# Kernel optimization log

Hardware: AMD Instinct MI355X
Metric: run time of the kernel (lower is better)

## Reference

```python
import jax, jax.numpy as jnp
import numpy as np

N = 32       # number of variables (per-var LSTMs)
L = 128      # window length
D = 128      # hidden dim
HEADS = 8
TAU_MAX = 5
ALPHA = 0.7  # attn_decay_alpha
B = 128      # number of time-ordered windows


def setup_inputs() -> dict:
    key = jax.random.key(0)
    ks = jax.random.split(key, 20)
    s = 0.1
    f = lambda k, shape: (jax.random.normal(k, shape, jnp.float32) * s)
    return {
        "X": jax.random.normal(ks[0], (B, L, N), jnp.float32),
        # per-variable encoder LSTM (input size 1): W_ih (N,4D), W_hh (N,4D,D), combined-style biases kept separate
        "enc_Wih": f(ks[1], (N, 4 * D)),
        "enc_Whh": f(ks[2], (N, 4 * D, D)),
        "enc_b": f(ks[3], (N, 4 * D)),            # b_ih + b_hh merged (mathematically identical)
        "pool_w": f(ks[4], (N, D)),
        "pool_b": f(ks[5], (N,)),
        # shared MultiheadAttention params (torch layout: in_proj (3D,D))
        "in_proj_w": f(ks[6], (3 * D, D)),
        "in_proj_b": f(ks[7], (3 * D,)),
        "out_proj_w": f(ks[8], (D, D)),
        "out_proj_b": f(ks[9], (D,)),
        # per-variable decoder: init_h/init_c Linear(d,d), LSTM(1,d) (input is all-zeros so W_ih drops out), out Linear(d,1)
        "dec_initH_w": f(ks[10], (N, D, D)),
        "dec_initH_b": f(ks[11], (N, D)),
        "dec_initC_w": f(ks[12], (N, D, D)),
        "dec_initC_b": f(ks[13], (N, D)),
        "dec_Whh": f(ks[14], (N, 4 * D, D)),
        "dec_bih": f(ks[15], (N, 4 * D)),
        "dec_bhh": f(ks[16], (N, 4 * D)),
        "dec_out_w": f(ks[17], (N, D)),
        "dec_out_b": f(ks[18], (N,)),
    }


def _lstm_cell(gates, c):
    # torch gate order: i, f, g, o
    i, fg, g, o = jnp.split(gates, 4, axis=-1)
    i = jax.nn.sigmoid(i); fg = jax.nn.sigmoid(fg)
    g = jnp.tanh(g); o = jax.nn.sigmoid(o)
    c = fg * c + i * g
    h = o * jnp.tanh(c)
    return h, c


def _encode(X, Wih, Whh, b, pool_w, pool_b):
    # X: (B,L,N); encoder consumes first L-1 steps of each variable, batched over all N vars
    x = jnp.transpose(X[:, :-1, :], (1, 2, 0))  # (T, N, B)
    Bn = X.shape[0]
    h0 = jnp.zeros((N, Bn, D), X.dtype)

    def step(carry, x_t):  # x_t: (N,B)
        h, c = carry
        gates = (x_t[..., None] * Wih[:, None, :]
                 + jnp.einsum('nbd,ngd->nbg', h, Whh)
                 + b[:, None, :])
        h, c = _lstm_cell(gates, c)
        return (h, c), h

    _, H = jax.lax.scan(step, (h0, h0), x)  # H: (T,N,B,D)
    # TemporalAttnPool: softmax over time of a linear score, weighted sum
    scores = jnp.einsum('tnbd,nd->tnb', H, pool_w) + pool_b[None, :, None]
    a = jax.nn.softmax(scores, axis=0)
    C = jnp.einsum('tnb,tnbd->bnd', a, H)  # (B,N,D)
    return C


def _mha(Q, KV, in_w, in_b, out_w, out_b):
    dh = D // HEADS
    q = Q @ in_w[:D].T + in_b[:D]
    k = KV @ in_w[D:2 * D].T + in_b[D:2 * D]
    v = KV @ in_w[2 * D:].T + in_b[2 * D:]
    sp = lambda x: x.reshape(x.shape[0], x.shape[1], HEADS, dh)
    q, k, v = sp(q), sp(k), sp(v)
    scores = jnp.einsum('bqhd,bkhd->bhqk', q, k) / float(np.sqrt(dh))
    attn = jax.nn.softmax(scores, axis=-1)
    o = jnp.einsum('bhqk,bkhd->bqhd', attn, v).reshape(Q.shape)
    return o @ out_w.T + out_b


def _cross_attend(C, in_w, in_b, out_w, out_b):
    Bn = C.shape[0]
    tmax = min(TAU_MAX, Bn - 1)
    if tmax <= 0:
        return C
    out_sum = jnp.zeros_like(C)
    w_sum = jnp.zeros((Bn, 1, 1), C.dtype)
    for tau in range(1, tmax + 1):  # small fixed loop over lags
        o = _mha(C[tau:], C[:-tau], in_w, in_b, out_w, out_b)
        w = float(np.exp(-ALPHA * (tau - 1)))  # attn_agg == 'decay'
        out_sum = out_sum.at[tau:].add(o * w)
        w_sum = w_sum.at[tau:].add(w)
    out = out_sum / jnp.clip(w_sum, 1e-8)
    return C + out  # residual=True


def _decode(C_star, iHw, iHb, iCw, iCb, Whh, bih, bhh, ow, ob):
    # h0/c0 from tanh(Linear(c_star)); LSTM input is all-zeros so input term reduces to b_ih
    h0 = jnp.tanh(jnp.einsum('bnd,ned->nbe', C_star, iHw) + iHb[:, None, :])
    c0 = jnp.tanh(jnp.einsum('bnd,ned->nbe', C_star, iCw) + iCb[:, None, :])
    b = (bih + bhh)[:, None, :]  # (N,1,4D)

    def step(carry, _):
        h, c = carry
        gates = jnp.einsum('nbd,ngd->nbg', h, Whh) + b
        h, c = _lstm_cell(gates, c)
        o = jnp.einsum('nbd,nd->nb', h, ow) + ob[:, None]
        return (h, c), o

    _, O = jax.lax.scan(step, (h0, c0), None, length=L)  # (L,N,B)
    recon = jnp.transpose(O[:L - 1], (2, 0, 1))  # (B,L-1,N)
    pred = O[L - 1].T                            # (B,N)
    return recon, pred


def reference(X, enc_Wih, enc_Whh, enc_b, pool_w, pool_b,
              in_proj_w, in_proj_b, out_proj_w, out_proj_b,
              dec_initH_w, dec_initH_b, dec_initC_w, dec_initC_b,
              dec_Whh, dec_bih, dec_bhh, dec_out_w, dec_out_b):
    C = _encode(X, enc_Wih, enc_Whh, enc_b, pool_w, pool_b)
    C_star = _cross_attend(C, in_proj_w, in_proj_b, out_proj_w, out_proj_b)
    recon, pred = _decode(C_star, dec_initH_w, dec_initH_b, dec_initC_w, dec_initC_b,
                          dec_Whh, dec_bih, dec_bhh, dec_out_w, dec_out_b)
    return recon, pred, C_star
```

## Files before the change

### kernel.cpp

```cpp
#include <hip/hip_runtime.h>
#include <hip/hip_bf16.h>

typedef unsigned short ushort_t;
typedef unsigned int uint_t;

#define DD   128
#define G4   512
#define BT   16
#define NB   128
#define NV   32

#define OFF_WIH   0
#define OFF_EB    16384
#define OFF_PW    32768
#define OFF_PB    36864
#define OFF_INW   36896
#define OFF_INB   86048
#define OFF_OUTW  86432
#define OFF_OUTB  102816
#define OFF_IHB   102944
#define OFF_ICB   107040
#define OFF_DBIH  111136
#define OFF_DBHH  127520
#define OFF_DOW   143904
#define OFF_DOB   148000
#define P_TOTAL   148032

typedef __attribute__((ext_vector_type(8))) short bf16x8;
typedef __attribute__((ext_vector_type(4))) float f32x4;

__device__ __forceinline__ float bf2f(ushort_t u) {
    union { uint_t i; float f; } x; x.i = ((uint_t)u) << 16; return x.f;
}
__device__ __forceinline__ ushort_t f2bf(float f) {
    __hip_bfloat16 h = __float2bfloat16(f);
    return *(ushort_t*)&h;
}
__device__ __forceinline__ uint_t f2u(float f) {
    union { float f; uint_t i; } x; x.f = f; return x.i;
}
__device__ __forceinline__ float u2f(uint_t u) {
    union { uint_t i; float f; } x; x.i = u; return x.f;
}
__device__ __forceinline__ float sigmoid_f(float x) {
    return __builtin_amdgcn_rcpf(1.f + __expf(-x));
}
__device__ __forceinline__ float tanh_f(float x) {
    float e = __expf(2.f * x);
    return 1.f - 2.f * __builtin_amdgcn_rcpf(e + 1.f);
}
__device__ __forceinline__ float swz_bcast_l15(float v) {
    return u2f((uint_t)__builtin_amdgcn_ds_swizzle((int)f2u(v), 0x000F));
}
__device__ __forceinline__ void store_out(void* out, long idx, float v, int bf) {
    if (bf) ((ushort_t*)out)[idx] = f2bf(v);
    else    ((float*)out)[idx]    = v;
}

struct Ptr19 { const void* p[19]; int e[19]; };

__global__ __launch_bounds__(64) void probe_kernel(Ptr19 a, int* __restrict__ flags) {
    int i = blockIdx.x;
    int t = threadIdx.x;
    int cap = a.e[i] < 2048 ? a.e[i] : 2048;
    int cnt = 0, tot = 0;
    const ushort_t* p = (const ushort_t*)a.p[i];
    for (int j = t; j < cap; j += 64) {
        ushort_t u = p[j];
        float af = fabsf(bf2f(u));
        tot++;
        if (u == 0 || (af > 1e-7f && af < 100.f)) cnt++;
    }
    #pragma unroll
    for (int off = 32; off >= 1; off >>= 1) {
        cnt += __shfl_xor(cnt, off);
        tot += __shfl_xor(tot, off);
    }
    if (t == 0) flags[i] = (cnt * 10 >= tot * 9) ? 1 : 0;
}

__global__ __launch_bounds__(256) void conv_all(Ptr19 a, const int* __restrict__ flags,
                                                float* __restrict__ P) {
    int i = blockIdx.x * 256 + threadIdx.x;
    if (i >= P_TOTAL) return;
    int src, off;
    if      (i < OFF_EB)   { src = 1;  off = i - OFF_WIH; }
    else if (i < OFF_PW)   { src = 3;  off = i - OFF_EB; }
    else if (i < OFF_PB)   { src = 4;  off = i - OFF_PW; }
    else if (i < OFF_INW)  { src = 5;  off = i - OFF_PB; }
    else if (i < OFF_INB)  { src = 6;  off = i - OFF_INW; }
    else if (i < OFF_OUTW) { src = 7;  off = i - OFF_INB; }
    else if (i < OFF_OUTB) { src = 8;  off = i - OFF_OUTW; }
    else if (i < OFF_IHB)  { src = 9;  off = i - OFF_OUTB; }
    else if (i < OFF_ICB)  { src = 11; off = i - OFF_IHB; }
    else if (i < OFF_DBIH) { src = 13; off = i - OFF_ICB; }
    else if (i < OFF_DBHH) { src = 15; off = i - OFF_DBIH; }
    else if (i < OFF_DOW)  { src = 16; off = i - OFF_DBHH; }
    else if (i < OFF_DOB)  { src = 17; off = i - OFF_DOW; }
    else                   { src = 18; off = i - OFF_DOB; }
    int bf = flags[src];
    P[i] = bf ? bf2f(((const ushort_t*)a.p[src])[off]) : ((const float*)a.p[src])[off];
}

__global__ __launch_bounds__(256) void transpose_X(const void* __restrict__ src,
                                                   const int* __restrict__ flags,
                                                   float* __restrict__ Xc) {
    __shared__ float tile[32][65];
    int bt  = blockIdx.x * 32;
    int tn0 = blockIdx.y * 64;
    int bf = flags[0];
    int tx = threadIdx.x & 63, ty = threadIdx.x >> 6;
    #pragma unroll
    for (int k = 0; k < 8; k++) {
        int row = ty * 8 + k;
        int idx = (bt + row) * 4096 + tn0 + tx;
        tile[row][tx] = bf ? bf2f(((const ushort_t*)src)[idx]) : ((const float*)src)[idx];
    }
    __syncthreads();
    int bx = threadIdx.x & 31, tyy = threadIdx.x >> 5;
    #pragma unroll
    for (int k = 0; k < 8; k++) {
        int tn = tn0 + tyy * 8 + k;
        int t = tn >> 5, nn = tn & 31;
        Xc[t * 4096 + nn * 128 + bt + bx] = tile[bx][tyy * 8 + k];
    }
}

__global__ __launch_bounds__(512, 2) void enc_kernel(
    const float* __restrict__ Xc, const void* __restrict__ Wraw,
    const int* __restrict__ flags, const float* __restrict__ P,
    float* __restrict__ Cout)
{
    const int n = blockIdx.y, b0 = blockIdx.x * BT;
    const int tid = threadIdx.x;
    const int w = tid >> 6, lane = tid & 63;
    const int l15 = lane & 15, quad = lane >> 4;
    const int wbf = flags[2];
    const int bown = b0 + l15;

    __shared__ alignas(16) ushort_t hS[2][16 * 136];
    for (int i = tid; i < 16 * 136; i += 512) hS[0][i] = 0;

    bf16x8 afrag[4][4];
    #pragma unroll
    for (int typ = 0; typ < 4; typ++) {
        const int g = typ * 128 + 16 * w + l15;
        #pragma unroll
        for (int kc = 0; kc < 4; kc++) {
            const int base = (n * G4 + g) * DD + 32 * kc + 8 * quad;
            if (wbf) {
                afrag[typ][kc] = *(const bf16x8*)((const ushort_t*)Wraw + base);
            } else {
                const float* fp = (const float*)Wraw + base;
                bf16x8 tmp;
                #pragma unroll
                for (int j = 0; j < 8; j++) tmp[j] = (short)f2bf(fp[j]);
                afrag[typ][kc] = tmp;
            }
        }
    }

    bf16x8 pfrag[4];
    #pragma unroll
    for (int kc = 0; kc < 4; kc++) {
        bf16x8 tmp;
        #pragma unroll
        for (int j = 0; j < 8; j++)
            tmp[j] = (l15 == 0 || l15 == 8)
                   ? (short)f2bf(P[OFF_PW + n * DD + 32 * kc + 8 * quad + j]) : (short)0;
        pfrag[kc] = tmp;
    }

    f32x4 bias4[4], wih4[4];
    #pragma unroll
    for (int typ = 0; typ < 4; typ++) {
        int base = n * G4 + typ * 128 + 16 * w + 4 * quad;
        bias4[typ] = *(const f32x4*)&P[OFF_EB + base];
        wih4[typ]  = *(const f32x4*)&P[OFF_WIH + base];
    }
    const float pb_r = P[OFF_PB + n];

    float cst[4], hprev[4], Cacc[4], lR = 0.f;
    #pragma unroll
    for (int r = 0; r < 4; r++) { cst[r] = 0.f; hprev[r] = 0.f; Cacc[r] = 0.f; }

    float xq = Xc[n * 128 + bown];

#define ENC_STEP(T, RB)                                                              \
    do {                                                                             \
        __syncthreads();                                                             \
        bf16x8 bh[4];                                                                \
        _Pragma("unroll")                                                            \
        for (int kc = 0; kc < 4; kc++)                                               \
            bh[kc] = *(const bf16x8*)&hS[RB][l15 * 136 + 32 * kc + 8 * quad];        \
        f32x4 acc[4], accP;                                                          \
        _Pragma("unroll")                                                            \
        for (int typ = 0; typ < 4; typ++) {                                          \
            f32x4 a;                                                                 \
            a.x = bias4[typ].x + xq * wih4[typ].x;                                   \
            a.y = bias4[typ].y + xq * wih4[typ].y;                                   \
            a.z = bias4[typ].z + xq * wih4[typ].z;                                   \
            a.w = bias4[typ].w + xq * wih4[typ].w;                                   \
            acc[typ] = a;                                                            \
        }                                                                            \
        accP.x = pb_r; accP.y = pb_r; accP.z = pb_r; accP.w = pb_r;                  \
        if ((T) < 126) xq = Xc[((T) + 1) * 4096 + n * 128 + bown];                   \
        _Pragma("unroll")                                                            \
        for (int kc = 0; kc < 4; kc++) {                                             \
            accP = __builtin_amdgcn_mfma_f32_16x16x32_bf16(pfrag[kc], bh[kc], accP, 0, 0, 0); \
            _Pragma("unroll")                                                        \
            for (int typ = 0; typ < 4; typ++)                                        \
                acc[typ] = __builtin_amdgcn_mfma_f32_16x16x32_bf16(afrag[typ][kc], bh[kc], acc[typ], 0, 0, 0); \
        }                                                                            \
        if ((T) > 0) {                                                               \
            float e = __expf(swz_bcast_l15(accP[0]));                                \
            lR += e;                                                                 \
            _Pragma("unroll")                                                        \
            for (int r = 0; r < 4; r++) Cacc[r] = fmaf(e, hprev[r], Cacc[r]);        \
        }                                                                            \
        ushort4 hw;                                                                  \
        _Pragma("unroll")                                                            \
        for (int r = 0; r < 4; r++) {                                                \
            float ii = sigmoid_f(acc[0][r]);                                         \
            float ff = sigmoid_f(acc[1][r]);                                         \
            float g2 = tanh_f(acc[2][r]);                                            \
            float oo = sigmoid_f(acc[3][r]);                                         \
            float cc = ff * cst[r] + ii * g2;                                        \
            cst[r] = cc;                                                             \
            float hh = oo * tanh_f(cc);                                              \
            hprev[r] = hh;                                                           \
            ((ushort_t*)&hw)[r] = f2bf(hh);                                          \
        }                                                                            \
        *(ushort4*)&hS[(RB) ^ 1][l15 * 136 + 16 * w + 4 * quad] = hw;                \
    } while (0)

    for (int tp = 0; tp < 63; tp++) {
        ENC_STEP(2 * tp, 0);
        ENC_STEP(2 * tp + 1, 1);
    }
    ENC_STEP(126, 0);
#undef ENC_STEP

    __syncthreads();
    {
        f32x4 accP;
        accP.x = pb_r; accP.y = pb_r; accP.z = pb_r; accP.w = pb_r;
        #pragma unroll
        for (int kc = 0; kc < 4; kc++) {
            bf16x8 bh = *(const bf16x8*)&hS[1][l15 * 136 + 32 * kc + 8 * quad];
            accP = __builtin_amdgcn_mfma_f32_16x16x32_bf16(pfrag[kc], bh, accP, 0, 0, 0);
        }
        float e = __expf(swz_bcast_l15(accP[0]));
        lR += e;
        #pragma unroll
        for (int r = 0; r < 4; r++) Cacc[r] = fmaf(e, hprev[r], Cacc[r]);
    }
    float inv = 1.f / lR;
    f32x4 cv;
    cv.x = Cacc[0] * inv; cv.y = Cacc[1] * inv; cv.z = Cacc[2] * inv; cv.w = Cacc[3] * inv;
    *(f32x4*)&Cout[bown * (NV * DD) + n * DD + 16 * w + 4 * quad] = cv;
}

__global__ __launch_bounds__(256) void qkv_kernel(
    const float* __restrict__ C, const float* __restrict__ P,
    float* __restrict__ q, float* __restrict__ k, float* __restrict__ v)
{
    int b = blockIdx.x, p = blockIdx.y, tid = threadIdx.x;
    int j = tid & 127, half = tid >> 7;
    __shared__ float Cb[NV * DD];
    for (int i = tid; i < NV * DD; i += 256) Cb[i] = C[b * (NV * DD) + i];
    __syncthreads();

    const float* wrow = P + OFF_INW + (p * DD + j) * DD;
    float bias = P[OFF_INB + p * DD + j];
    float acc[16];
    #pragma unroll
    for (int nn = 0; nn < 16; nn++) acc[nn] = bias;

    for (int dc = 0; dc < DD; dc += 8) {
        float4 w0 = *(const float4*)&wrow[dc];
        float4 w1 = *(const float4*)&wrow[dc + 4];
        #pragma unroll
        for (int nn = 0; nn < 16; nn++) {
            const float* cb = &Cb[(half * 16 + nn) * DD + dc];
            float4 c0 = *(float4*)&cb[0];
            float4 c1 = *(float4*)&cb[4];
            acc[nn] += c0.x * w0.x + c0.y * w0.y + c0.z * w0.z + c0.w * w0.w
                     + c1.x * w1.x + c1.y * w1.y + c1.z * w1.z + c1.w * w1.w;
        }
    }
    float* dst = (p == 0) ? q : (p == 1) ? k : v;
    for (int nn = 0; nn < 16; nn++)
        dst[b * (NV * DD) + (half * 16 + nn) * DD + j] = acc[nn];
}

__global__ __launch_bounds__(256) void attn_kernel(
    const float* __restrict__ q, const float* __restrict__ k, const float* __restrict__ v,
    const float* __restrict__ C, const float* __restrict__ P,
    const int* __restrict__ flags, float* __restrict__ Cstar, void* __restrict__ dout)
{
    int b = blockIdx.x, tid = threadIdx.x;
    int obf = flags[0];
    __shared__ float Qs[NV * DD], Ks[NV * DD], Vs[NV * DD];
    float* Os = Ks;
    for (int i = tid; i < NV * DD; i += 256) Qs[i] = q[b * (NV * DD) + i];
    __syncthreads();

    int hh = tid >> 5, qi = tid & 31;
    float qreg[16];
    #pragma unroll
    for (int u = 0; u < 4; u++) {
        float4 t4 = *(float4*)&Qs[qi * DD + hh * 16 + 4 * u];
        qreg[4*u] = t4.x; qreg[4*u+1] = t4.y; qreg[4*u+2] = t4.z; qreg[4*u+3] = t4.w;
    }

    float Oacc[16];
    #pragma unroll
    for (int u = 0; u < 16; u++) Oacc[u] = 0.f;
    float wsum = 0.f;
    int tmax = (b < 5) ? b : 5;

    for (int tau = 1; tau <= tmax; tau++) {
        __syncthreads();
        for (int i = tid; i < NV * DD; i += 256) {
            Ks[i] = k[(b - tau) * (NV * DD) + i];
            Vs[i] = v[(b - tau) * (NV * DD) + i];
        }
        __syncthreads();

        float s[NV];
        #pragma unroll
        for (int kk = 0; kk < NV; kk++) {
            float a = 0.f;
            #pragma unroll
            for (int u = 0; u < 4; u++) {
                float4 kv = *(float4*)&Ks[kk * DD + hh * 16 + 4 * u];
                a += qreg[4*u] * kv.x + qreg[4*u+1] * kv.y
                   + qreg[4*u+2] * kv.z + qreg[4*u+3] * kv.w;
            }
            s[kk] = a * 0.25f;
        }
        float mm = s[0];
        #pragma unroll
        for (int kk = 1; kk < NV; kk++) mm = fmaxf(mm, s[kk]);
        float ssum = 0.f;
        #pragma unroll
        for (int kk = 0; kk < NV; kk++) { s[kk] = __expf(s[kk] - mm); ssum += s[kk]; }
        float wdk = __expf(-0.7f * (float)(tau - 1));
        wsum += wdk;
        float wr = wdk / ssum;
        #pragma unroll
        for (int u = 0; u < 4; u++) {
            float ax = 0.f, ay = 0.f, az = 0.f, aw = 0.f;
            #pragma unroll
            for (int kk = 0; kk < NV; kk++) {
                float4 vv = *(float4*)&Vs[kk * DD + hh * 16 + 4 * u];
                ax += s[kk] * vv.x; ay += s[kk] * vv.y;
                az += s[kk] * vv.z; aw += s[kk] * vv.w;
            }
            Oacc[4*u] += wr * ax; Oacc[4*u+1] += wr * ay;
            Oacc[4*u+2] += wr * az; Oacc[4*u+3] += wr * aw;
        }
    }

    __syncthreads();
    float winv = (b > 0) ? 1.f / wsum : 0.f;
    #pragma unroll
    for (int u = 0; u < 16; u++)
        Os[qi * DD + hh * 16 + u] = Oacc[u] * winv;
    __syncthreads();

    int j = tid & 127, ng = tid >> 7;
    const float* wrow = P + OFF_OUTW + j * DD;
    float obias = P[OFF_OUTB + j];
    for (int nn = ng * 16; nn < ng * 16 + 16; nn++) {
        float a = (b > 0) ? obias : 0.f;
        for (int dc = 0; dc < DD; dc += 8) {
            float4 w0 = *(const float4*)&wrow[dc];
            float4 w1 = *(const float4*)&wrow[dc + 4];
            float4 o0 = *(float4*)&Os[nn * DD + dc];
            float4 o1 = *(float4*)&Os[nn * DD + dc + 4];
            a += o0.x*w0.x + o0.y*w0.y + o0.z*w0.z + o0.w*w0.w
               + o1.x*w1.x + o1.y*w1.y + o1.z*w1.z + o1.w*w1.w;
        }
        float cs = C[b * (NV * DD) + nn * DD + j] + a;
        Cstar[b * (NV * DD) + nn * DD + j] = cs;
        store_out(dout, 524288 + b * (NV * DD) + nn * DD + j, cs, obf);
    }
}

__global__ __launch_bounds__(512, 2) void dec_kernel(
    const float* __restrict__ Cstar,
    const void* __restrict__ iHw, const void* __restrict__ iCw,
    const void* __restrict__ Wraw, const int* __restrict__ flags,
    const float* __restrict__ P, void* __restrict__ out)
{
    const int n = blockIdx.y, b0 = blockIdx.x * BT;
    const int tid = threadIdx.x;
    const int w = tid >> 6, lane = tid & 63;
    const int l15 = lane & 15, quad = lane >> 4;
    const int wbf = flags[14], obf = flags[0];
    const int bown = b0 + l15;

    __shared__ alignas(16) ushort_t hS[2][16 * 136];

    bf16x8 cstB[4];
    #pragma unroll
    for (int kc = 0; kc < 4; kc++) {
        const float* cp = &Cstar[bown * (NV * DD) + n * DD + 32 * kc + 8 * quad];
        f32x4 c0v = *(const f32x4*)&cp[0];
        f32x4 c1v = *(const f32x4*)&cp[4];
        bf16x8 tmp;
        tmp[0] = (short)f2bf(c0v.x); tmp[1] = (short)f2bf(c0v.y);
        tmp[2] = (short)f2bf(c0v.z); tmp[3] = (short)f2bf(c0v.w);
        tmp[4] = (short)f2bf(c1v.x); tmp[5] = (short)f2bf(c1v.y);
        tmp[6] = (short)f2bf(c1v.z); tmp[7] = (short)f2bf(c1v.w);
        cstB[kc] = tmp;
    }
    float cst[4];
    {
        const int hbf = flags[10], cbf = flags[12];
        f32x4 hAcc = *(const f32x4*)&P[OFF_IHB + n * DD + 16 * w + 4 * quad];
        f32x4 cAcc = *(const f32x4*)&P[OFF_ICB + n * DD + 16 * w + 4 * quad];
        #pragma unroll
        for (int kc = 0; kc < 4; kc++) {
            const int base = (n * DD + 16 * w + l15) * DD + 32 * kc + 8 * quad;
            bf16x8 wA;
            if (hbf) wA = *(const bf16x8*)((const ushort_t*)iHw + base);
            else {
                const float* fp = (const float*)iHw + base;
                #pragma unroll
                for (int j = 0; j < 8; j++) wA[j] = (short)f2bf(fp[j]);
            }
            hAcc = __builtin_amdgcn_mfma_f32_16x16x32_bf16(wA, cstB[kc], hAcc, 0, 0, 0);
            if (cbf) wA = *(const bf16x8*)((const ushort_t*)iCw + base);
            else {
                const float* fp = (const float*)iCw + base;
                #pragma unroll
                for (int j = 0; j < 8; j++) wA[j] = (short)f2bf(fp[j]);
            }
            cAcc = __builtin_amdgcn_mfma_f32_16x16x32_bf16(wA, cstB[kc], cAcc, 0, 0, 0);
        }
        ushort4 hw;
        #pragma unroll
        for (int r = 0; r < 4; r++) {
            ((ushort_t*)&hw)[r] = f2bf(tanh_f(hAcc[r]));
            cst[r] = tanh_f(cAcc[r]);
        }
        *(ushort4*)&hS[0][l15 * 136 + 16 * w + 4 * quad] = hw;
    }

    bf16x8 afrag[4][4];
    #pragma unroll
    for (int typ = 0; typ < 4; typ++) {
        const int g = typ * 128 + 16 * w + l15;
        #pragma unroll
        for (int kc = 0; kc < 4; kc++) {
            const int base = (n * G4 + g) * DD + 32 * kc + 8 * quad;
            if (wbf) {
                afrag[typ][kc] = *(const bf16x8*)((const ushort_t*)Wraw + base);
            } else {
                const float* fp = (const float*)Wraw + base;
                bf16x8 tmp;
                #pragma unroll
                for (int j = 0; j < 8; j++) tmp[j] = (short)f2bf(fp[j]);
                afrag[typ][kc] = tmp;
            }
        }
    }

    bf16x8 pfrag[4];
    #pragma unroll
    for (int kc = 0; kc < 4; kc++) {
        bf16x8 tmp;
        #pragma unroll
        for (int j = 0; j < 8; j++)
            tmp[j] = (l15 == 0) ? (short)f2bf(P[OFF_DOW + n * DD + 32 * kc + 8 * quad + j]) : (short)0;
        pfrag[kc] = tmp;
    }

    f32x4 bias4[4];
    #pragma unroll
    for (int typ = 0; typ < 4; typ++) {
        int base = n * G4 + typ * 128 + 16 * w + 4 * quad;
        f32x4 b1 = *(const f32x4*)&P[OFF_DBIH + base];
        f32x4 b2 = *(const f32x4*)&P[OFF_DBHH + base];
        bias4[typ].x = b1.x + b2.x; bias4[typ].y = b1.y + b2.y;
        bias4[typ].z = b1.z + b2.z; bias4[typ].w = b1.w + b2.w;
    }
    const float ob_r = P[OFF_DOB + n];

#define DEC_STEP(T, RB)                                                              \
    do {                                                                             \
        __syncthreads();                                                             \
        bf16x8 bh[4];                                                                \
        _Pragma("unroll")                                                            \
        for (int kc = 0; kc < 4; kc++)                                               \
            bh[kc] = *(const bf16x8*)&hS[RB][l15 * 136 + 32 * kc + 8 * quad];        \
        f32x4 acc[4];                                                                \
        _Pragma("unroll")                                                            \
        for (int typ = 0; typ < 4; typ++) acc[typ] = bias4[typ];                     \
        _Pragma("unroll")                                                            \
        for (int kc = 0; kc < 4; kc++)                                               \
            _Pragma("unroll")                                                        \
            for (int typ = 0; typ < 4; typ++)                                        \
                acc[typ] = __builtin_amdgcn_mfma_f32_16x16x32_bf16(afrag[typ][kc], bh[kc], acc[typ], 0, 0, 0); \
        if (w == 0) {                                                                \
            f32x4 accP;                                                              \
            accP.x = ob_r; accP.y = ob_r; accP.z = ob_r; accP.w = ob_r;              \
            _Pragma("unroll")                                                        \
            for (int kc = 0; kc < 4; kc++)                                           \
                accP = __builtin_amdgcn_mfma_f32_16x16x32_bf16(pfrag[kc], bh[kc], accP, 0, 0, 0); \
            if ((T) > 0 && quad == 0)                                                \
                store_out(out, (long)bown * 4064 + (long)((T) - 1) * NV + n, accP[0], obf); \
        }                                                                            \
        ushort4 hw;                                                                  \
        _Pragma("unroll")                                                            \
        for (int r = 0; r < 4; r++) {                                                \
            float ii = sigmoid_f(acc[0][r]);                                         \
            float ff = sigmoid_f(acc[1][r]);                                         \
            float g2 = tanh_f(acc[2][r]);                                            \
            float oo = sigmoid_f(acc[3][r]);                                         \
            float cc = ff * cst[r] + ii * g2;                                        \
            cst[r] = cc;                                                             \
            ((ushort_t*)&hw)[r] = f2bf(oo * tanh_f(cc));                             \
        }                                                                            \
        *(ushort4*)&hS[(RB) ^ 1][l15 * 136 + 16 * w + 4 * quad] = hw;                \
    } while (0)

    for (int tp = 0; tp < 64; tp++) {
        DEC_STEP(2 * tp, 0);
        DEC_STEP(2 * tp + 1, 1);
    }
#undef DEC_STEP

    __syncthreads();
    if (w == 0) {
        f32x4 accP;
        accP.x = ob_r; accP.y = ob_r; accP.z = ob_r; accP.w = ob_r;
        #pragma unroll
        for (int kc = 0; kc < 4; kc++) {
            bf16x8 bh = *(const bf16x8*)&hS[0][l15 * 136 + 32 * kc + 8 * quad];
            accP = __builtin_amdgcn_mfma_f32_16x16x32_bf16(pfrag[kc], bh, accP, 0, 0, 0);
        }
        if (quad == 0)
            store_out(out, 520192 + (long)bown * NV + n, accP[0], obf);
    }
}

extern "C" void kernel_launch(void* const* d_in, const int* in_sizes, int n_in,
                              void* d_out, int out_size, void* d_ws, size_t ws_size,
                              hipStream_t stream) {
    char* ws = (char*)d_ws;
    float*    P    = (float*)(ws + 0);
    float*    Xc   = (float*)(ws + (1u << 20));
    float*    C    = (float*)(ws + (3u << 20));
    float*    qb   = (float*)(ws + (5u << 20));
    float*    kb   = (float*)(ws + (7u << 20));
    float*    vb   = (float*)(ws + (9u << 20));
    float*    Cst  = (float*)(ws + (11u << 20));
    int*      flags = (int*)(ws + (13u << 20));

    Ptr19 a;
    for (int i = 0; i < 19; i++) { a.p[i] = d_in[i]; a.e[i] = in_sizes[i]; }
    probe_kernel<<<19, 64, 0, stream>>>(a, flags);
    conv_all<<<(P_TOTAL + 255) / 256, 256, 0, stream>>>(a, flags, P);
    transpose_X<<<dim3(4, 64), 256, 0, stream>>>(d_in[0], flags, Xc);

    enc_kernel<<<dim3(8, 32), 512, 0, stream>>>(Xc, d_in[2], flags, P, C);
    qkv_kernel<<<dim3(128, 3), 256, 0, stream>>>(C, P, qb, kb, vb);
    attn_kernel<<<dim3(128), 256, 0, stream>>>(qb, kb, vb, C, P, flags, Cst, d_out);
    dec_kernel<<<dim3(8, 32), 512, 0, stream>>>(Cst, d_in[10], d_in[12], d_in[14], flags, P, d_out);
}
```

Before: 435.3 us.

## Fuse prep kernels, move QKV projection into encoder, and merge LSTM cell reciprocals

Merges the probe, parameter-conversion and X-transpose kernels into one prep kernel. Each kernel now detects the input dtype itself with a per-wave probe instead of reading a flags buffer. The QKV projection is folded into the encoder epilogue, working from a shared-memory copy of C, so the separate qkv kernel launch is removed. The LSTM cell shares reciprocals across gate pairs to cut rcp instructions on the recurrent critical path. The cost is redundant probing reads in every block and a scalar-FMA QKV stage inside the encoder.

```diff
diff --git a/kernel.cpp b/kernel.cpp
--- a/kernel.cpp
+++ b/kernel.cpp
@@ -14,17 +14,17 @@
 #define OFF_EB    16384
 #define OFF_PW    32768
 #define OFF_PB    36864
-#define OFF_INW   36896
-#define OFF_INB   86048
-#define OFF_OUTW  86432
-#define OFF_OUTB  102816
-#define OFF_IHB   102944
-#define OFF_ICB   107040
-#define OFF_DBIH  111136
-#define OFF_DBHH  127520
-#define OFF_DOW   143904
-#define OFF_DOB   148000
-#define P_TOTAL   148032
+#define OFF_INW   37120
+#define OFF_INB   86272
+#define OFF_OUTW  86784
+#define OFF_OUTB  103168
+#define OFF_IHB   103424
+#define OFF_ICB   107520
+#define OFF_DBIH  111616
+#define OFF_DBHH  128000
+#define OFF_DOW   144384
+#define OFF_DOB   148480
+#define P_TOTAL   148736
 
 typedef __attribute__((ext_vector_type(8))) short bf16x8;
 typedef __attribute__((ext_vector_type(4))) float f32x4;
@@ -42,13 +42,26 @@
 __device__ __forceinline__ float u2f(uint_t u) {
     union { uint_t i; float f; } x; x.i = u; return x.f;
 }
-__device__ __forceinline__ float sigmoid_f(float x) {
-    return __builtin_amdgcn_rcpf(1.f + __expf(-x));
-}
 __device__ __forceinline__ float tanh_f(float x) {
     float e = __expf(2.f * x);
     return 1.f - 2.f * __builtin_amdgcn_rcpf(e + 1.f);
 }
+__device__ __forceinline__ float lstm_cell(float gi, float gf, float gg, float go, float& c) {
+    float ei = __expf(-gi), ef = __expf(-gf);
+    float di = 1.f + ei, df = 1.f + ef;
+    float r1 = __builtin_amdgcn_rcpf(di * df);
+    float ii = df * r1;
+    float ff = di * r1;
+    float eg = __expf(-2.f * gg), eo = __expf(-go);
+    float dg = 1.f + eg, dz = 1.f + eo;
+    float r2 = __builtin_amdgcn_rcpf(dg * dz);
+    float oo = dg * r2;
+    float tg = (1.f - eg) * (dz * r2);
+    c = ff * c + ii * tg;
+    float ec = __expf(-2.f * c);
+    float tc = (1.f - ec) * __builtin_amdgcn_rcpf(1.f + ec);
+    return oo * tc;
+}
 __device__ __forceinline__ float swz_bcast_l15(float v) {
     return u2f((uint_t)__builtin_amdgcn_ds_swizzle((int)f2u(v), 0x000F));
 }
@@ -56,89 +69,89 @@
     if (bf) ((ushort_t*)out)[idx] = f2bf(v);
     else    ((float*)out)[idx]    = v;
 }
-
-struct Ptr19 { const void* p[19]; int e[19]; };
-
-__global__ __launch_bounds__(64) void probe_kernel(Ptr19 a, int* __restrict__ flags) {
-    int i = blockIdx.x;
-    int t = threadIdx.x;
-    int cap = a.e[i] < 2048 ? a.e[i] : 2048;
+__device__ __forceinline__ int wave_probe(const void* p, int elems) {
+    int cap = elems < 2048 ? elems : 2048;
+    int lane = threadIdx.x & 63;
+    const ushort_t* u = (const ushort_t*)p;
     int cnt = 0, tot = 0;
-    const ushort_t* p = (const ushort_t*)a.p[i];
-    for (int j = t; j < cap; j += 64) {
-        ushort_t u = p[j];
-        float af = fabsf(bf2f(u));
+    for (int j = lane; j < cap; j += 64) {
+        ushort_t x = u[j];
+        float af = fabsf(bf2f(x));
         tot++;
-        if (u == 0 || (af > 1e-7f && af < 100.f)) cnt++;
+        if (x == 0 || (af > 1e-7f && af < 100.f)) cnt++;
     }
     #pragma unroll
     for (int off = 32; off >= 1; off >>= 1) {
         cnt += __shfl_xor(cnt, off);
         tot += __shfl_xor(tot, off);
     }
-    if (t == 0) flags[i] = (cnt * 10 >= tot * 9) ? 1 : 0;
-}
-
-__global__ __launch_bounds__(256) void conv_all(Ptr19 a, const int* __restrict__ flags,
-                                                float* __restrict__ P) {
-    int i = blockIdx.x * 256 + threadIdx.x;
-    if (i >= P_TOTAL) return;
-    int src, off;
-    if      (i < OFF_EB)   { src = 1;  off = i - OFF_WIH; }
-    else if (i < OFF_PW)   { src = 3;  off = i - OFF_EB; }
-    else if (i < OFF_PB)   { src = 4;  off = i - OFF_PW; }
-    else if (i < OFF_INW)  { src = 5;  off = i - OFF_PB; }
-    else if (i < OFF_INB)  { src = 6;  off = i - OFF_INW; }
-    else if (i < OFF_OUTW) { src = 7;  off = i - OFF_INB; }
-    else if (i < OFF_OUTB) { src = 8;  off = i - OFF_OUTW; }
-    else if (i < OFF_IHB)  { src = 9;  off = i - OFF_OUTB; }
-    else if (i < OFF_ICB)  { src = 11; off = i - OFF_IHB; }
-    else if (i < OFF_DBIH) { src = 13; off = i - OFF_ICB; }
-    else if (i < OFF_DBHH) { src = 15; off = i - OFF_DBIH; }
-    else if (i < OFF_DOW)  { src = 16; off = i - OFF_DBHH; }
-    else if (i < OFF_DOB)  { src = 17; off = i - OFF_DOW; }
-    else                   { src = 18; off = i - OFF_DOB; }
-    int bf = flags[src];
-    P[i] = bf ? bf2f(((const ushort_t*)a.p[src])[off]) : ((const float*)a.p[src])[off];
-}
-
-__global__ __launch_bounds__(256) void transpose_X(const void* __restrict__ src,
-                                                   const int* __restrict__ flags,
+    return (cnt * 10 >= tot * 9) ? 1 : 0;
+}
+
+struct Ptr19 { const void* p[19]; };
+
+__global__ __launch_bounds__(256) void prep_kernel(Ptr19 a, float* __restrict__ P,
                                                    float* __restrict__ Xc) {
     __shared__ float tile[32][65];
-    int bt  = blockIdx.x * 32;
-    int tn0 = blockIdx.y * 64;
-    int bf = flags[0];
-    int tx = threadIdx.x & 63, ty = threadIdx.x >> 6;
-    #pragma unroll
-    for (int k = 0; k < 8; k++) {
-        int row = ty * 8 + k;
-        int idx = (bt + row) * 4096 + tn0 + tx;
-        tile[row][tx] = bf ? bf2f(((const ushort_t*)src)[idx]) : ((const float*)src)[idx];
-    }
-    __syncthreads();
-    int bx = threadIdx.x & 31, tyy = threadIdx.x >> 5;
-    #pragma unroll
-    for (int k = 0; k < 8; k++) {
-        int tn = tn0 + tyy * 8 + k;
-        int t = tn >> 5, nn = tn & 31;
-        Xc[t * 4096 + nn * 128 + bt + bx] = tile[bx][tyy * 8 + k];
+    if (blockIdx.x < 581) {
+        int base = blockIdx.x * 256;
+        int src, o0, size;
+        if      (base < OFF_EB)   { src = 1;  o0 = base - OFF_WIH;  size = 16384; }
+        else if (base < OFF_PW)   { src = 3;  o0 = base - OFF_EB;   size = 16384; }
+        else if (base < OFF_PB)   { src = 4;  o0 = base - OFF_PW;   size = 4096;  }
+        else if (base < OFF_INW)  { src = 5;  o0 = base - OFF_PB;   size = 32;    }
+        else if (base < OFF_INB)  { src = 6;  o0 = base - OFF_INW;  size = 49152; }
+        else if (base < OFF_OUTW) { src = 7;  o0 = base - OFF_INB;  size = 384;   }
+        else if (base < OFF_OUTB) { src = 8;  o0 = base - OFF_OUTW; size = 16384; }
+        else if (base < OFF_IHB)  { src = 9;  o0 = base - OFF_OUTB; size = 128;   }
+        else if (base < OFF_ICB)  { src = 11; o0 = base - OFF_IHB;  size = 4096;  }
+        else if (base < OFF_DBIH) { src = 13; o0 = base - OFF_ICB;  size = 4096;  }
+        else if (base < OFF_DBHH) { src = 15; o0 = base - OFF_DBIH; size = 16384; }
+        else if (base < OFF_DOW)  { src = 16; o0 = base - OFF_DBHH; size = 16384; }
+        else if (base < OFF_DOB)  { src = 17; o0 = base - OFF_DOW;  size = 4096;  }
+        else                      { src = 18; o0 = base - OFF_DOB;  size = 32;    }
+        int bf = wave_probe(a.p[src], size);
+        int off = o0 + (int)threadIdx.x;
+        if (off < size)
+            P[base + threadIdx.x] = bf ? bf2f(((const ushort_t*)a.p[src])[off])
+                                       : ((const float*)a.p[src])[off];
+    } else {
+        int bf = wave_probe(a.p[0], 2048);
+        int idx2 = blockIdx.x - 581;
+        int bt = (idx2 & 3) * 32, tn0 = (idx2 >> 2) * 64;
+        const void* src = a.p[0];
+        int tx = threadIdx.x & 63, ty = threadIdx.x >> 6;
+        #pragma unroll
+        for (int k = 0; k < 8; k++) {
+            int row = ty * 8 + k;
+            int idx = (bt + row) * 4096 + tn0 + tx;
+            tile[row][tx] = bf ? bf2f(((const ushort_t*)src)[idx]) : ((const float*)src)[idx];
+        }
+        __syncthreads();
+        int bx = threadIdx.x & 31, tyy = threadIdx.x >> 5;
+        #pragma unroll
+        for (int k = 0; k < 8; k++) {
+            int tn = tn0 + tyy * 8 + k;
+            int t = tn >> 5, nn = tn & 31;
+            Xc[t * 4096 + nn * 128 + bt + bx] = tile[bx][tyy * 8 + k];
+        }
     }
 }
 
 __global__ __launch_bounds__(512, 2) void enc_kernel(
     const float* __restrict__ Xc, const void* __restrict__ Wraw,
-    const int* __restrict__ flags, const float* __restrict__ P,
-    float* __restrict__ Cout)
+    const float* __restrict__ P, float* __restrict__ Cout,
+    float* __restrict__ q, float* __restrict__ k, float* __restrict__ v)
 {
     const int n = blockIdx.y, b0 = blockIdx.x * BT;
     const int tid = threadIdx.x;
     const int w = tid >> 6, lane = tid & 63;
     const int l15 = lane & 15, quad = lane >> 4;
-    const int wbf = flags[2];
     const int bown = b0 + l15;
+    const int wbf = wave_probe(Wraw, 2048);
 
     __shared__ alignas(16) ushort_t hS[2][16 * 136];
+    __shared__ alignas(16) float Cs[16 * 132];
     for (int i = tid; i < 16 * 136; i += 512) hS[0][i] = 0;
 
     bf16x8 afrag[4][4];
@@ -221,13 +234,7 @@
         ushort4 hw;                                                                  \
         _Pragma("unroll")                                                            \
         for (int r = 0; r < 4; r++) {                                                \
-            float ii = sigmoid_f(acc[0][r]);                                         \
-            float ff = sigmoid_f(acc[1][r]);                                         \
-            float g2 = tanh_f(acc[2][r]);                                            \
-            float oo = sigmoid_f(acc[3][r]);                                         \
-            float cc = ff * cst[r] + ii * g2;                                        \
-            cst[r] = cc;                                                             \
-            float hh = oo * tanh_f(cc);                                              \
+            float hh = lstm_cell(acc[0][r], acc[1][r], acc[2][r], acc[3][r], cst[r]);\
             hprev[r] = hh;                                                           \
             ((ushort_t*)&hw)[r] = f2bf(hh);                                          \
         }                                                                            \
@@ -255,52 +262,59 @@
         #pragma unroll
         for (int r = 0; r < 4; r++) Cacc[r] = fmaf(e, hprev[r], Cacc[r]);
     }
-    float inv = 1.f / lR;
+    float inv = __builtin_amdgcn_rcpf(lR);
     f32x4 cv;
     cv.x = Cacc[0] * inv; cv.y = Cacc[1] * inv; cv.z = Cacc[2] * inv; cv.w = Cacc[3] * inv;
     *(f32x4*)&Cout[bown * (NV * DD) + n * DD + 16 * w + 4 * quad] = cv;
-}
-
-__global__ __launch_bounds__(256) void qkv_kernel(
-    const float* __restrict__ C, const float* __restrict__ P,
-    float* __restrict__ q, float* __restrict__ k, float* __restrict__ v)
-{
-    int b = blockIdx.x, p = blockIdx.y, tid = threadIdx.x;
-    int j = tid & 127, half = tid >> 7;
-    __shared__ float Cb[NV * DD];
-    for (int i = tid; i < NV * DD; i += 256) Cb[i] = C[b * (NV * DD) + i];
+    #pragma unroll
+    for (int r = 0; r < 4; r++)
+        Cs[l15 * 132 + 16 * w + 4 * quad + r] = Cacc[r] * inv;
     __syncthreads();
 
-    const float* wrow = P + OFF_INW + (p * DD + j) * DD;
-    float bias = P[OFF_INB + p * DD + j];
-    float acc[16];
-    #pragma unroll
-    for (int nn = 0; nn < 16; nn++) acc[nn] = bias;
-
-    for (int dc = 0; dc < DD; dc += 8) {
-        float4 w0 = *(const float4*)&wrow[dc];
-        float4 w1 = *(const float4*)&wrow[dc + 4];
-        #pragma unroll
-        for (int nn = 0; nn < 16; nn++) {
-            const float* cb = &Cb[(half * 16 + nn) * DD + dc];
-            float4 c0 = *(float4*)&cb[0];
-            float4 c1 = *(float4*)&cb[4];
-            acc[nn] += c0.x * w0.x + c0.y * w0.y + c0.z * w0.z + c0.w * w0.w
-                     + c1.x * w1.x + c1.y * w1.y + c1.z * w1.z + c1.w * w1.w;
-        }
-    }
-    float* dst = (p == 0) ? q : (p == 1) ? k : v;
-    for (int nn = 0; nn < 16; nn++)
-        dst[b * (NV * DD) + (half * 16 + nn) * DD + j] = acc[nn];
+    {
+        int bb = tid >> 5, col = tid & 31;
+        const float* crow = &Cs[bb * 132];
+        float acc[12];
+        #pragma unroll
+        for (int p3 = 0; p3 < 3; p3++)
+            #pragma unroll
+            for (int u = 0; u < 4; u++)
+                acc[p3 * 4 + u] = P[OFF_INB + p3 * DD + col + 32 * u];
+        for (int dc = 0; dc < DD; dc += 16) {
+            f32x4 c0 = *(const f32x4*)&crow[dc];
+            f32x4 c1 = *(const f32x4*)&crow[dc + 4];
+            f32x4 c2 = *(const f32x4*)&crow[dc + 8];
+            f32x4 c3 = *(const f32x4*)&crow[dc + 12];
+            #pragma unroll
+            for (int m = 0; m < 12; m++) {
+                int j = (m >> 2) * DD + col + 32 * (m & 3);
+                const float* wr = &P[OFF_INW + j * DD + dc];
+                f32x4 w0 = *(const f32x4*)&wr[0];
+                f32x4 w1 = *(const f32x4*)&wr[4];
+                f32x4 w2 = *(const f32x4*)&wr[8];
+                f32x4 w3 = *(const f32x4*)&wr[12];
+                acc[m] += c0.x*w0.x + c0.y*w0.y + c0.z*w0.z + c0.w*w0.w
+                        + c1.x*w1.x + c1.y*w1.y + c1.z*w1.z + c1.w*w1.w
+                        + c2.x*w2.x + c2.y*w2.y + c2.z*w2.z + c2.w*w2.w
+                        + c3.x*w3.x + c3.y*w3.y + c3.z*w3.z + c3.w*w3.w;
+            }
+        }
+        #pragma unroll
+        for (int m = 0; m < 12; m++) {
+            int p3 = m >> 2, j = col + 32 * (m & 3);
+            float* dst = (p3 == 0) ? q : (p3 == 1) ? k : v;
+            dst[(b0 + bb) * (NV * DD) + n * DD + j] = acc[m];
+        }
+    }
 }
 
 __global__ __launch_bounds__(256) void attn_kernel(
     const float* __restrict__ q, const float* __restrict__ k, const float* __restrict__ v,
     const float* __restrict__ C, const float* __restrict__ P,
-    const int* __restrict__ flags, float* __restrict__ Cstar, void* __restrict__ dout)
+    const void* __restrict__ Xraw, float* __restrict__ Cstar, void* __restrict__ dout)
 {
     int b = blockIdx.x, tid = threadIdx.x;
-    int obf = flags[0];
+    int obf = wave_probe(Xraw, 2048);
     __shared__ float Qs[NV * DD], Ks[NV * DD], Vs[NV * DD];
     float* Os = Ks;
     for (int i = tid; i < NV * DD; i += 256) Qs[i] = q[b * (NV * DD) + i];
@@ -392,22 +406,24 @@
 __global__ __launch_bounds__(512, 2) void dec_kernel(
     const float* __restrict__ Cstar,
     const void* __restrict__ iHw, const void* __restrict__ iCw,
-    const void* __restrict__ Wraw, const int* __restrict__ flags,
+    const void* __restrict__ Wraw, const void* __restrict__ Xraw,
     const float* __restrict__ P, void* __restrict__ out)
 {
     const int n = blockIdx.y, b0 = blockIdx.x * BT;
     const int tid = threadIdx.x;
     const int w = tid >> 6, lane = tid & 63;
     const int l15 = lane & 15, quad = lane >> 4;
-    const int wbf = flags[14], obf = flags[0];
-    const int bown = b0 + l15;
+    const int wbf = wave_probe(Wraw, 2048);
+    const int obf = wave_probe(Xraw, 2048);
+    const int hbf = wave_probe(iHw, 2048);
+    const int cbf = wave_probe(iCw, 2048);
 
     __shared__ alignas(16) ushort_t hS[2][16 * 136];
 
     bf16x8 cstB[4];
     #pragma unroll
     for (int kc = 0; kc < 4; kc++) {
-        const float* cp = &Cstar[bown * (NV * DD) + n * DD + 32 * kc + 8 * quad];
+        const float* cp = &Cstar[(b0 + l15) * (NV * DD) + n * DD + 32 * kc + 8 * quad];
         f32x4 c0v = *(const f32x4*)&cp[0];
         f32x4 c1v = *(const f32x4*)&cp[4];
         bf16x8 tmp;
@@ -419,7 +435,6 @@
     }
     float cst[4];
     {
-        const int hbf = flags[10], cbf = flags[12];
         f32x4 hAcc = *(const f32x4*)&P[OFF_IHB + n * DD + 16 * w + 4 * quad];
         f32x4 cAcc = *(const f32x4*)&P[OFF_ICB + n * DD + 16 * w + 4 * quad];
         #pragma unroll
@@ -489,6 +504,7 @@
         bias4[typ].z = b1.z + b2.z; bias4[typ].w = b1.w + b2.w;
     }
     const float ob_r = P[OFF_DOB + n];
+    const int bown = b0 + l15;
 
 #define DEC_STEP(T, RB)                                                              \
     do {                                                                             \
@@ -516,15 +532,8 @@
         }                                                                            \
         ushort4 hw;                                                                  \
         _Pragma("unroll")                                                            \
-        for (int r = 0; r < 4; r++) {                                                \
-            float ii = sigmoid_f(acc[0][r]);                                         \
-            float ff = sigmoid_f(acc[1][r]);                                         \
-            float g2 = tanh_f(acc[2][r]);                                            \
-            float oo = sigmoid_f(acc[3][r]);                                         \
-            float cc = ff * cst[r] + ii * g2;                                        \
-            cst[r] = cc;                                                             \
-            ((ushort_t*)&hw)[r] = f2bf(oo * tanh_f(cc));                             \
-        }                                                                            \
+        for (int r = 0; r < 4; r++)                                                  \
+            ((ushort_t*)&hw)[r] = f2bf(lstm_cell(acc[0][r], acc[1][r], acc[2][r], acc[3][r], cst[r])); \
         *(ushort4*)&hS[(RB) ^ 1][l15 * 136 + 16 * w + 4 * quad] = hw;                \
     } while (0)
 
@@ -559,16 +568,12 @@
     float*    kb   = (float*)(ws + (7u << 20));
     float*    vb   = (float*)(ws + (9u << 20));
     float*    Cst  = (float*)(ws + (11u << 20));
-    int*      flags = (int*)(ws + (13u << 20));
 
     Ptr19 a;
-    for (int i = 0; i < 19; i++) { a.p[i] = d_in[i]; a.e[i] = in_sizes[i]; }
-    probe_kernel<<<19, 64, 0, stream>>>(a, flags);
-    conv_all<<<(P_TOTAL + 255) / 256, 256, 0, stream>>>(a, flags, P);
-    transpose_X<<<dim3(4, 64), 256, 0, stream>>>(d_in[0], flags, Xc);
-
-    enc_kernel<<<dim3(8, 32), 512, 0, stream>>>(Xc, d_in[2], flags, P, C);
-    qkv_kernel<<<dim3(128, 3), 256, 0, stream>>>(C, P, qb, kb, vb);
-    attn_kernel<<<dim3(128), 256, 0, stream>>>(qb, kb, vb, C, P, flags, Cst, d_out);
-    dec_kernel<<<dim3(8, 32), 512, 0, stream>>>(Cst, d_in[10], d_in[12], d_in[14], flags, P, d_out);
-}
+    for (int i = 0; i < 19; i++) a.p[i] = d_in[i];
+
+    prep_kernel<<<837, 256, 0, stream>>>(a, P, Xc);
+    enc_kernel<<<dim3(8, 32), 512, 0, stream>>>(Xc, d_in[2], P, C, qb, kb, vb);
+    attn_kernel<<<128, 256, 0, stream>>>(qb, kb, vb, C, P, d_in[0], Cst, d_out);
+    dec_kernel<<<dim3(8, 32), 512, 0, stream>>>(Cst, d_in[10], d_in[12], d_in[14], d_in[0], P, d_out);
+}
```

After: 513.7 us. 1.18x slower.
